# Kernel tuning notes

Hardware: AMD Instinct MI355X
Metric: run time of the kernel (lower is better)

Reference implementation:

```python
import jax, jax.numpy as jnp
import numpy as np

C_IN = 256
C_INTER = 128


def _pool_tv(a):
    # max-pool by 2 over the last two dims (t, v); kernel (1,2,2)
    *lead, t, v = a.shape
    return a.reshape(*lead, t // 2, 2, v // 2, 2).max(axis=(-3, -1))


def setup_inputs() -> dict:
    key = jax.random.key(0)
    ks = jax.random.split(key, 9)
    b, c, views, t, v = 8, 512, 4, 32, 32
    s = 1.0 / np.sqrt(C_IN)
    si = 1.0 / np.sqrt(C_INTER)
    return {
        "x": jax.random.normal(ks[0], (b, c, views, t, v), dtype=jnp.float32),
        "g_w": jax.random.normal(ks[1], (C_INTER, C_IN), dtype=jnp.float32) * s,
        "g_b": jax.random.normal(ks[2], (C_INTER,), dtype=jnp.float32) * s,
        "theta_w": jax.random.normal(ks[3], (C_INTER, C_IN), dtype=jnp.float32) * s,
        "theta_b": jax.random.normal(ks[4], (C_INTER,), dtype=jnp.float32) * s,
        "phi_w": jax.random.normal(ks[5], (C_INTER, C_IN), dtype=jnp.float32) * s,
        "phi_b": jax.random.normal(ks[6], (C_INTER,), dtype=jnp.float32) * s,
        "W_w": jax.random.normal(ks[7], (C_IN, C_INTER), dtype=jnp.float32) * si,
        "W_b": jax.random.normal(ks[8], (C_IN,), dtype=jnp.float32) * si,
    }


def reference(x, g_w, g_b, theta_w, theta_b, phi_w, phi_b, W_w, W_b):
    b, c, views, t, v = x.shape
    G = c // C_IN  # channel groups
    x5 = x.reshape(b, C_IN, G, views, t, v)
    x_pool = x5.mean(axis=2)  # (b, C_IN, views, t, v)

    # g branch: per-group 1x1 conv then (1,2,2) max-pool
    x_g = jnp.swapaxes(x5, 1, 2)  # (b, G, C_IN, views, t, v)
    g_full = jnp.einsum('bgcvtw,oc->bgovtw', x_g, g_w) + g_b[None, None, :, None, None, None]
    g_pooled = _pool_tv(g_full)  # (b, G, inter, views, t/2, v/2)
    M = views * (t // 2) * (v // 2)
    # (b, G, inter, M) -> (b, inter, G, M) -> (b, inter*G, M) -> (b, M, inter*G)
    g_x = jnp.swapaxes(g_pooled.reshape(b, G, C_INTER, M), 1, 2).reshape(b, C_INTER * G, M)
    g_x = jnp.swapaxes(g_x, 1, 2)

    # theta on full-resolution pooled-over-group x; phi subsampled
    N = views * t * v
    theta_x = jnp.einsum('bcvtw,oc->bovtw', x_pool, theta_w) + theta_b[None, :, None, None, None]
    theta_x = jnp.swapaxes(theta_x.reshape(b, C_INTER, N), 1, 2)  # (b, N, inter)
    phi_full = jnp.einsum('bcvtw,oc->bovtw', x_pool, phi_w) + phi_b[None, :, None, None, None]
    phi_x = _pool_tv(phi_full).reshape(b, C_INTER, M)  # (b, inter, M)

    f = jnp.einsum('bni,bim->bnm', theta_x, phi_x)  # (b, N, M)
    f_div_C = jax.nn.softmax(f, axis=-1)
    y = jnp.einsum('bnm,bmd->bnd', f_div_C, g_x)  # (b, N, inter*G)

    # (b, inter*G, N) -> (b, inter, G, views, t, v) -> (b, G, inter, ...)
    y = jnp.swapaxes(y, 1, 2).reshape(b, C_INTER, G, views, t, v)
    y = jnp.swapaxes(y, 1, 2)
    W_y = jnp.einsum('bgivtw,oi->bgovtw', y, W_w) + W_b[None, None, :, None, None, None]
    W_y = jnp.swapaxes(W_y, 1, 2).reshape(b, c, views, t, v)
    return W_y + x
```

## Files before the change

### kernel.cpp

```cpp
#include <hip/hip_runtime.h>

#define F_Y     0u
#define F_TH    4194304u
#define F_PHIB  6291456u
#define F_GB    6815744u

typedef __attribute__((ext_vector_type(4))) float f32x4;
typedef __attribute__((ext_vector_type(8))) short bf16x8;

__device__ __forceinline__ unsigned short f2bf(float f) {
  union { unsigned int i; float f; } x; x.f = f;
  unsigned int r = x.i + 0x7fffu + ((x.i >> 16) & 1u);
  return (unsigned short)(r >> 16);
}
__device__ __forceinline__ unsigned int pk2(float a, float b) {
  return (unsigned int)f2bf(a) | ((unsigned int)f2bf(b) << 16);
}
__device__ __forceinline__ void gload_lds16(const void* g, void* l) {
  __builtin_amdgcn_global_load_lds(
      (const __attribute__((address_space(1))) unsigned int*)g,
      (__attribute__((address_space(3))) unsigned int*)l, 16, 0, 0);
}

__global__ __launch_bounds__(512)
void k_front(const float* __restrict__ x,
             const float* __restrict__ tw, const float* __restrict__ tb,
             const float* __restrict__ pw, const float* __restrict__ pb,
             const float* __restrict__ gw, const float* __restrict__ gb,
             float* __restrict__ ws) {
  const int nt = blockIdx.x, b = blockIdx.y;
  const int n0 = nt * 128;
  const int tid = threadIdx.x;
  const int w = tid >> 6, lane = tid & 63, q = lane >> 4, col = lane & 15;

  __shared__ uint4 ldsb[5888];
  char* lds = (char*)ldsb;
  char* xs  = lds;
  char* Xm  = lds + 32768;
  char* Xg0 = lds + 43008;
  char* Xg1 = lds + 53248;
  char* Wt  = lds + 63488;
  char* Wp  = lds + 73728;
  char* Wg  = lds + 83968;

  f32x4 at[8], ap[8], a0[8], a1[8];
#pragma unroll
  for (int j = 0; j < 8; ++j) {
    at[j] = (f32x4){0.f, 0.f, 0.f, 0.f};
    ap[j] = (f32x4){0.f, 0.f, 0.f, 0.f};
    a0[j] = (f32x4){0.f, 0.f, 0.f, 0.f};
    a1[j] = (f32x4){0.f, 0.f, 0.f, 0.f};
  }

  for (int kc = 0; kc < 8; ++kc) {
    {
      const int ch = tid >> 5;
      const int so = (tid & 31) * 16;
#pragma unroll
      for (int i = 0; i < 4; ++i) {
        const int chh = 16 * i + ch;
        const float* src = x + ((size_t)(b * 512 + 64 * kc + chh)) * 4096 + n0;
        gload_lds16((const char*)src + (so ^ ((chh & 7) << 4)),
                    xs + 8192 * i + tid * 16);
      }
      const int o = tid >> 2, c4 = tid & 3;
      const size_t wo = (size_t)o * 256 + 32 * kc + 8 * c4;
      float4 t0 = ((const float4*)(tw + wo))[0], t1 = ((const float4*)(tw + wo))[1];
      float4 p0 = ((const float4*)(pw + wo))[0], p1 = ((const float4*)(pw + wo))[1];
      float4 g0 = ((const float4*)(gw + wo))[0], g1 = ((const float4*)(gw + wo))[1];
      *(uint4*)(Wt + o * 80 + 16 * c4) =
          make_uint4(pk2(t0.x, t0.y), pk2(t0.z, t0.w), pk2(t1.x, t1.y), pk2(t1.z, t1.w));
      *(uint4*)(Wp + o * 80 + 16 * c4) =
          make_uint4(pk2(p0.x, p0.y), pk2(p0.z, p0.w), pk2(p1.x, p1.y), pk2(p1.z, p1.w));
      *(uint4*)(Wg + o * 80 + 16 * c4) =
          make_uint4(pk2(g0.x, g0.y), pk2(g0.z, g0.w), pk2(g1.x, g1.y), pk2(g1.z, g1.w));
    }
    __syncthreads();
    {
      const int n = tid >> 2, c4 = tid & 3;
      unsigned um[4], u0[4], u1[4];
#pragma unroll
      for (int s = 0; s < 4; ++s) {
        float v[4];
#pragma unroll
        for (int e = 0; e < 2; ++e) {
          const int cp = 8 * c4 + 2 * s + e;
          const int l0 = 2 * cp, l1 = 2 * cp + 1;
          v[2 * e]     = *(const float*)(xs + l0 * 512 + ((n * 4) ^ ((l0 & 7) << 4)));
          v[2 * e + 1] = *(const float*)(xs + l1 * 512 + ((n * 4) ^ ((l1 & 7) << 4)));
        }
        um[s] = pk2(0.5f * (v[0] + v[1]), 0.5f * (v[2] + v[3]));
        u0[s] = pk2(v[0], v[2]);
        u1[s] = pk2(v[1], v[3]);
      }
      *(uint4*)(Xm  + n * 80 + 16 * c4) = make_uint4(um[0], um[1], um[2], um[3]);
      *(uint4*)(Xg0 + n * 80 + 16 * c4) = make_uint4(u0[0], u0[1], u0[2], u0[3]);
      *(uint4*)(Xg1 + n * 80 + 16 * c4) = make_uint4(u1[0], u1[1], u1[2], u1[3]);
    }
    __syncthreads();
    {
      const int ar = 16 * w + col;
      const bf16x8 aft = *(const bf16x8*)(Wt + ar * 80 + 16 * q);
      const bf16x8 afp = *(const bf16x8*)(Wp + ar * 80 + 16 * q);
      const bf16x8 afg = *(const bf16x8*)(Wg + ar * 80 + 16 * q);
#pragma unroll
      for (int j = 0; j < 8; ++j) {
        const int br = 16 * j + col;
        const bf16x8 bm = *(const bf16x8*)(Xm  + br * 80 + 16 * q);
        const bf16x8 b0 = *(const bf16x8*)(Xg0 + br * 80 + 16 * q);
        const bf16x8 b1 = *(const bf16x8*)(Xg1 + br * 80 + 16 * q);
        at[j] = __builtin_amdgcn_mfma_f32_16x16x32_bf16(aft, bm, at[j], 0, 0, 0);
        ap[j] = __builtin_amdgcn_mfma_f32_16x16x32_bf16(afp, bm, ap[j], 0, 0, 0);
        a0[j] = __builtin_amdgcn_mfma_f32_16x16x32_bf16(afg, b0, a0[j], 0, 0, 0);
        a1[j] = __builtin_amdgcn_mfma_f32_16x16x32_bf16(afg, b1, a1[j], 0, 0, 0);
      }
    }
    __syncthreads();
  }

  const int o0 = 16 * w + 4 * q;
  const int mb = (nt >> 3) * 256 + (nt & 7) * 32;

  {
    float bst[4];
#pragma unroll
    for (int r = 0; r < 4; ++r) bst[r] = tb[o0 + r];
#pragma unroll
    for (int j = 0; j < 8; ++j) {
      const int n = 16 * j + col;
      uint2 pkk = make_uint2(pk2(at[j][0] + bst[0], at[j][1] + bst[1]),
                             pk2(at[j][2] + bst[2], at[j][3] + bst[3]));
      *(uint2*)(xs + n * 256 + ((2 * o0) ^ ((n & 7) << 4))) = pkk;
    }
  }

  {
    float bsp[4];
#pragma unroll
    for (int r = 0; r < 4; ++r) bsp[r] = pb[o0 + r];
    unsigned short* phiB = (unsigned short*)(ws + F_PHIB);
#pragma unroll
    for (int jj = 0; jj < 4; ++jj) {
      const int j = (jj >> 1) * 4 + (jj & 1);
      f32x4 pm;
#pragma unroll
      for (int r = 0; r < 4; ++r) pm[r] = fmaxf(ap[j][r], ap[j + 2][r]);
#pragma unroll
      for (int r = 0; r < 4; ++r) pm[r] = fmaxf(pm[r], __shfl_xor(pm[r], 1));
      if ((col & 1) == 0) {
        const int vp = 8 * (j & 1) + (col >> 1);
        const int m = mb + 16 * (j >> 2) + vp;
        uint2 pkk = make_uint2(pk2(pm[0] + bsp[0], pm[1] + bsp[1]),
                               pk2(pm[2] + bsp[2], pm[3] + bsp[3]));
        *(uint2*)(phiB + ((size_t)(b * 1024) + m) * 128 + o0) = pkk;
      }
    }
  }

  {
    float bsg[4];
#pragma unroll
    for (int r = 0; r < 4; ++r) bsg[r] = gb[o0 + r];
#pragma unroll
    for (int gr = 0; gr < 2; ++gr) {
      char* pt = gr ? Xg1 : Xg0;
      const f32x4* ag = gr ? a1 : a0;
#pragma unroll
      for (int jj = 0; jj < 4; ++jj) {
        const int j = (jj >> 1) * 4 + (jj & 1);
        f32x4 pm;
#pragma unroll
        for (int r = 0; r < 4; ++r) pm[r] = fmaxf(ag[j][r], ag[j + 2][r]);
#pragma unroll
        for (int r = 0; r < 4; ++r) pm[r] = fmaxf(pm[r], __shfl_xor(pm[r], 1));
        if ((col & 1) == 0) {
          const int ml = 16 * (j >> 2) + 8 * (j & 1) + (col >> 1);
#pragma unroll
          for (int r = 0; r < 4; ++r)
            *(unsigned short*)(pt + (o0 + r) * 80 + ml * 2) = f2bf(pm[r] + bsg[r]);
        }
      }
    }
  }
  __syncthreads();

  {
    const int n = tid >> 2, seg = tid & 3;
    unsigned short* dst = (unsigned short*)(ws + F_TH) +
                          ((size_t)(b * 4096) + n0 + n) * 128 + seg * 32;
    const char* row = xs + n * 256;
    const int sw = (n & 7) << 4;
#pragma unroll
    for (int k = 0; k < 4; ++k)
      ((uint4*)dst)[k] = *(const uint4*)(row + ((64 * seg + 16 * k) ^ sw));
  }
  if (tid < 256) {
    const int o = tid >> 1, gr = tid & 1;
    const char* row = (gr ? Xg1 : Xg0) + o * 80;
    unsigned short* dst = (unsigned short*)(ws + F_GB) +
                          ((size_t)(b * 256) + 2 * o + gr) * 1024 + mb;
#pragma unroll
    for (int k = 0; k < 4; ++k)
      ((uint4*)dst)[k] = *(const uint4*)(row + 16 * k);
  }
}

#define NSIT 16
__global__ __launch_bounds__(512)
void k_attn_mfma(float* __restrict__ ws) {
  const int b = blockIdx.x;
  const int n0 = blockIdx.y * 128;
  const int tid = threadIdx.x;
  const int w = tid >> 6;
  const int lane = tid & 63;
  const int q = lane >> 4;
  const int col = lane & 15;
  const int ksw = (col & 7) << 4;

  __shared__ char lds[131072];
  char* plw0 = lds + 98304 + w * 4096;
  char* plw1 = plw0 + 2048;

  const unsigned short* thetaB = (const unsigned short*)(ws + F_TH);
  const char* phiBb = (const char*)((const unsigned short*)(ws + F_PHIB) + (size_t)b * 1024 * 128);
  const char* gBb   = (const char*)((const unsigned short*)(ws + F_GB) + (size_t)b * 256 * 1024);
  unsigned short* yB = (unsigned short*)(ws + F_Y);

  const int kr0 = lane >> 4;
  const int kso = (lane & 15) * 16;
  const int vr0 = lane >> 3;
  const int vso = (lane & 7) * 16;

  bf16x8 qf[4];
  {
    const unsigned short* qp = thetaB + ((size_t)(b * 4096 + n0 + 16 * w + col)) * 128 + 8 * q;
#pragma unroll
    for (int c = 0; c < 4; ++c) qf[c] = *(const bf16x8*)(qp + 32 * c);
  }

  f32x4 ot[16];
#pragma unroll
  for (int t = 0; t < 16; ++t) ot[t] = (f32x4){0.f, 0.f, 0.f, 0.f};
  float mrun = -1e30f, lsum = 0.f;

  {
    const int r = 4 * w + kr0;
    gload_lds16(phiBb + (size_t)r * 256 + (kso ^ ((r & 7) << 4)), lds + w * 1024);
    gload_lds16(phiBb + (size_t)(32 + r) * 256 + (kso ^ ((r & 7) << 4)),
                lds + 8192 + w * 1024);
#pragma unroll
    for (int j = 0; j < 4; ++j) {
      const int c = 4 * w + j;
      const int d = 8 * c + vr0;
      gload_lds16(gBb + (size_t)d * 2048 + (vso ^ ((d & 7) << 4)),
                  lds + 32768 + c * 1024);
    }
  }
  __syncthreads();

  for (int sit = 0; sit < NSIT; ++sit) {
    char* kt0 = lds + ((2 * sit) & 3) * 8192;
    char* kt1 = lds + ((2 * sit + 1) & 3) * 8192;
    char* vtc = lds + 32768 + (sit & 1) * 32768;

    if (sit + 1 < NSIT) {
      const int r = 4 * w + kr0;
      const int swk = (kso ^ ((r & 7) << 4));
      gload_lds16(phiBb + (size_t)((2 * sit + 2) * 32 + r) * 256 + swk,
                  lds + ((2 * sit + 2) & 3) * 8192 + w * 1024);
      gload_lds16(phiBb + (size_t)((2 * sit + 3) * 32 + r) * 256 + swk,
                  lds + ((2 * sit + 3) & 3) * 8192 + w * 1024);
      const size_t vm = (size_t)((sit + 1) * 64) * 2;
#pragma unroll
      for (int j = 0; j < 4; ++j) {
        const int c = 4 * w + j;
        const int d = 8 * c + vr0;
        gload_lds16(gBb + (size_t)d * 2048 + vm + (vso ^ ((d & 7) << 4)),
                    lds + 32768 + ((sit & 1) ^ 1) * 32768 + c * 1024);
      }
    }

    f32x4 st0[2], st1[2];
#pragma unroll
    for (int s = 0; s < 2; ++s) {
      st0[s] = (f32x4){0.f, 0.f, 0.f, 0.f};
      st1[s] = (f32x4){0.f, 0.f, 0.f, 0.f};
    }
    __builtin_amdgcn_s_setprio(1);
#pragma unroll
    for (int c = 0; c < 4; ++c)
#pragma unroll
      for (int s = 0; s < 2; ++s) {
        const bf16x8 kf0 = *(const bf16x8*)(kt0 + (16 * s + col) * 256 +
                                            ((64 * c + 16 * q) ^ ksw));
        const bf16x8 kf1 = *(const bf16x8*)(kt1 + (16 * s + col) * 256 +
                                            ((64 * c + 16 * q) ^ ksw));
        st0[s] = __builtin_amdgcn_mfma_f32_16x16x32_bf16(kf0, qf[c], st0[s], 0, 0, 0);
        st1[s] = __builtin_amdgcn_mfma_f32_16x16x32_bf16(kf1, qf[c], st1[s], 0, 0, 0);
      }
    __builtin_amdgcn_s_setprio(0);

    float pmax = -1e30f;
#pragma unroll
    for (int s = 0; s < 2; ++s)
#pragma unroll
      for (int r = 0; r < 4; ++r) {
        pmax = fmaxf(pmax, st0[s][r]);
        pmax = fmaxf(pmax, st1[s][r]);
      }
    pmax = fmaxf(pmax, __shfl_xor(pmax, 16));
    pmax = fmaxf(pmax, __shfl_xor(pmax, 32));
    if (!__all(pmax - mrun <= 8.f)) {
      const float mnew = fmaxf(mrun, pmax);
      const float scl = __expf(mrun - mnew);
      mrun = mnew;
      lsum *= scl;
#pragma unroll
      for (int t = 0; t < 16; ++t) {
        ot[t][0] *= scl; ot[t][1] *= scl; ot[t][2] *= scl; ot[t][3] *= scl;
      }
    }
    float rsum = 0.f;
#pragma unroll
    for (int s = 0; s < 2; ++s)
#pragma unroll
      for (int r = 0; r < 4; ++r) {
        st0[s][r] = __expf(st0[s][r] - mrun);
        st1[s][r] = __expf(st1[s][r] - mrun);
        rsum += st0[s][r] + st1[s][r];
      }
    rsum += __shfl_xor(rsum, 16);
    rsum += __shfl_xor(rsum, 32);
    lsum += rsum;

    char* prow0 = plw0 + col * 128;
    char* prow1 = plw1 + col * 128;
#pragma unroll
    for (int s = 0; s < 2; ++s)
#pragma unroll
      for (int hp = 0; hp < 2; ++hp) {
        *(unsigned int*)(prow0 + ((32 * s + 8 * q + 4 * hp) ^ ksw)) =
            pk2(st0[s][2 * hp], st0[s][2 * hp + 1]);
        *(unsigned int*)(prow1 + ((32 * s + 8 * q + 4 * hp) ^ ksw)) =
            pk2(st1[s][2 * hp], st1[s][2 * hp + 1]);
      }
    const bf16x8 pf0 = *(const bf16x8*)(prow0 + ((16 * q) ^ ksw));
    const bf16x8 pf1 = *(const bf16x8*)(prow1 + ((16 * q) ^ ksw));

    __builtin_amdgcn_s_setprio(1);
#pragma unroll
    for (int t = 0; t < 16; ++t) {
      const int d = 16 * t + col;
      const int dsw = (d & 7) << 4;
      const bf16x8 vf0 = *(const bf16x8*)(vtc + d * 128 + ((16 * q) ^ dsw));
      ot[t] = __builtin_amdgcn_mfma_f32_16x16x32_bf16(vf0, pf0, ot[t], 0, 0, 0);
    }
#pragma unroll
    for (int t = 0; t < 16; ++t) {
      const int d = 16 * t + col;
      const int dsw = (d & 7) << 4;
      const bf16x8 vf1 = *(const bf16x8*)(vtc + d * 128 + ((64 + 16 * q) ^ dsw));
      ot[t] = __builtin_amdgcn_mfma_f32_16x16x32_bf16(vf1, pf1, ot[t], 0, 0, 0);
    }
    __builtin_amdgcn_s_setprio(0);

    __syncthreads();
  }

  const float inv = 1.f / lsum;
  char* yt = lds;
  const int nl = 16 * w + col;
  const int swn = (nl & 7) << 4;
#pragma unroll
  for (int t = 0; t < 16; ++t) {
    const unsigned int w0 = pk2(ot[t][0] * inv, ot[t][2] * inv);
    const unsigned int w1 = pk2(ot[t][1] * inv, ot[t][3] * inv);
    const int bo = 16 * t + 4 * q;
    *(unsigned int*)(yt + nl * 256 + (bo ^ swn)) = w0;
    *(unsigned int*)(yt + (128 + nl) * 256 + (bo ^ swn)) = w1;
  }
  __syncthreads();
  {
    const int row = tid >> 1, h2 = tid & 1;
    const int gr = row >> 7, n = row & 127;
    unsigned short* dst = yB + (((size_t)(b * 2 + gr)) * 4096 + n0 + n) * 128 + h2 * 64;
    const char* srow = yt + row * 256;
    const int sw = (n & 7) << 4;
#pragma unroll
    for (int k = 0; k < 8; ++k)
      ((uint4*)dst)[k] = *(const uint4*)(srow + ((128 * h2 + 16 * k) ^ sw));
  }
}

__global__ __launch_bounds__(256)
void k_final_mfma(const float* __restrict__ x,
                  const float* __restrict__ Ww, const float* __restrict__ Wb,
                  const float* __restrict__ ws, float* __restrict__ out) {
  const int nt = blockIdx.x, gq = blockIdx.y, b = blockIdx.z;
  const int gr = gq & 1, ob = (gq >> 1) * 128;
  const int n0 = nt * 128;
  const int tid = threadIdx.x;
  const int w = tid >> 6, lane = tid & 63, q = lane >> 4, col = lane & 15;
  const unsigned short* yb = (const unsigned short*)(ws + F_Y);

  __shared__ uint4 ldsb[4096];
  char* As = (char*)ldsb;
  char* Bs = (char*)ldsb + 16384;

  f32x4 acc[2][8];
#pragma unroll
  for (int h = 0; h < 2; ++h)
#pragma unroll
    for (int j = 0; j < 8; ++j) acc[h][j] = (f32x4){0.f, 0.f, 0.f, 0.f};

  const int ro = tid >> 1, haf = tid & 1;
  for (int ks = 0; ks < 2; ++ks) {
    __syncthreads();
    {
      const float* src = Ww + (size_t)(ob + ro) * 128 + ks * 64 + haf * 32;
      char* row = As + ro * 128;
      const int sw = (ro & 7) << 4;
#pragma unroll
      for (int jj = 0; jj < 4; ++jj) {
        float4 a = ((const float4*)src)[2 * jj];
        float4 c4 = ((const float4*)src)[2 * jj + 1];
        uint4 pk;
        pk.x = pk2(a.x, a.y);  pk.y = pk2(a.z, a.w);
        pk.z = pk2(c4.x, c4.y); pk.w = pk2(c4.z, c4.w);
        *(uint4*)(row + ((haf * 64 + 16 * jj) ^ sw)) = pk;
      }
    }
    {
      const unsigned short* src = yb + (((size_t)(b * 2 + gr)) * 4096 + n0 + ro) * 128 + ks * 64 + haf * 32;
      char* row = Bs + ro * 128;
      const int sw = (ro & 7) << 4;
#pragma unroll
      for (int jj = 0; jj < 4; ++jj)
        *(uint4*)(row + ((haf * 64 + 16 * jj) ^ sw)) = ((const uint4*)src)[jj];
    }
    __syncthreads();
#pragma unroll
    for (int c = 0; c < 2; ++c) {
      bf16x8 af[2], bfr[8];
#pragma unroll
      for (int h = 0; h < 2; ++h) {
        const int r = 32 * w + 16 * h + col;
        af[h] = *(const bf16x8*)(As + r * 128 + ((64 * c + 16 * q) ^ ((r & 7) << 4)));
      }
#pragma unroll
      for (int j = 0; j < 8; ++j) {
        const int r = 16 * j + col;
        bfr[j] = *(const bf16x8*)(Bs + r * 128 + ((64 * c + 16 * q) ^ ((r & 7) << 4)));
      }
#pragma unroll
      for (int h = 0; h < 2; ++h)
#pragma unroll
        for (int j = 0; j < 8; ++j)
          acc[h][j] = __builtin_amdgcn_mfma_f32_16x16x32_bf16(af[h], bfr[j], acc[h][j], 0, 0, 0);
    }
  }

  __syncthreads();
  char* ft = (char*)ldsb;
#pragma unroll
  for (int h = 0; h < 2; ++h) {
    const int o0 = 32 * w + 16 * h + 4 * q;
#pragma unroll
    for (int j = 0; j < 8; ++j) {
      const int n = 16 * j + col;
#pragma unroll
      for (int r = 0; r < 4; ++r)
        *(float*)(ft + (o0 + r) * 512 + ((n * 4) ^ (((o0 + r) & 7) << 4))) = acc[h][j][r];
    }
  }
  __syncthreads();
  {
    const int o = tid >> 1, h2 = tid & 1;
    const float bsv = Wb[ob + o];
    const int ch = 2 * (ob + o) + gr;
    const size_t base = ((size_t)(b * 512 + ch)) * 4096 + n0 + h2 * 64;
    const char* row = ft + o * 512;
    const int sw = (o & 7) << 4;
#pragma unroll
    for (int k = 0; k < 16; ++k) {
      f32x4 v = *(const f32x4*)(row + ((256 * h2 + 16 * k) ^ sw));
      float4 xv = ((const float4*)(x + base))[k];
      ((float4*)(out + base))[k] = make_float4(v[0] + bsv + xv.x, v[1] + bsv + xv.y,
                                               v[2] + bsv + xv.z, v[3] + bsv + xv.w);
    }
  }
}

extern "C" void kernel_launch(void* const* d_in, const int* in_sizes, int n_in,
                              void* d_out, int out_size, void* d_ws, size_t ws_size,
                              hipStream_t stream) {
  const float* x  = (const float*)d_in[0];
  const float* gw = (const float*)d_in[1];
  const float* gb = (const float*)d_in[2];
  const float* tw = (const float*)d_in[3];
  const float* tb = (const float*)d_in[4];
  const float* pw = (const float*)d_in[5];
  const float* pb = (const float*)d_in[6];
  const float* Ww = (const float*)d_in[7];
  const float* Wb = (const float*)d_in[8];
  float* out = (float*)d_out;
  float* ws  = (float*)d_ws;

  k_front<<<dim3(32, 8), 512, 0, stream>>>(x, tw, tb, pw, pb, gw, gb, ws);
  k_attn_mfma<<<dim3(8, 32), 512, 0, stream>>>(ws);
  k_final_mfma<<<dim3(32, 4, 8), 256, 0, stream>>>(x, Ww, Wb, ws, out);
}
```

Measured before the change: 124.5 us.

## Fuse output W projection and residual into attention kernel epilogue

The final 1x1 W projection, bias and residual add move into the attention kernel's epilogue. The normalized y tile stays in LDS and each block multiplies it by W (read from global and converted to bf16 on the fly) with MFMA, then writes out+x directly. This removes the y workspace round trip and one kernel launch. In exchange the attention kernel carries 128 extra accumulator registers, which may reduce occupancy, and each block reloads the W weights from global memory without LDS staging.

```diff
diff --git a/kernel.cpp b/kernel.cpp
--- a/kernel.cpp
+++ b/kernel.cpp
@@ -1,9 +1,8 @@
 #include <hip/hip_runtime.h>
 
-#define F_Y     0u
-#define F_TH    4194304u
-#define F_PHIB  6291456u
-#define F_GB    6815744u
+#define F_TH    0u
+#define F_PHIB  2097152u
+#define F_GB    2621440u
 
 typedef __attribute__((ext_vector_type(4))) float f32x4;
 typedef __attribute__((ext_vector_type(8))) short bf16x8;
@@ -207,7 +206,9 @@
 
 #define NSIT 16
 __global__ __launch_bounds__(512)
-void k_attn_mfma(float* __restrict__ ws) {
+void k_attn_mfma(const float* __restrict__ x,
+                 const float* __restrict__ Ww, const float* __restrict__ Wb,
+                 float* __restrict__ ws, float* __restrict__ out) {
   const int b = blockIdx.x;
   const int n0 = blockIdx.y * 128;
   const int tid = threadIdx.x;
@@ -224,7 +225,6 @@
   const unsigned short* thetaB = (const unsigned short*)(ws + F_TH);
   const char* phiBb = (const char*)((const unsigned short*)(ws + F_PHIB) + (size_t)b * 1024 * 128);
   const char* gBb   = (const char*)((const unsigned short*)(ws + F_GB) + (size_t)b * 256 * 1024);
-  unsigned short* yB = (unsigned short*)(ws + F_Y);
 
   const int kr0 = lane >> 4;
   const int kso = (lane & 15) * 16;
@@ -369,125 +369,87 @@
 
   const float inv = 1.f / lsum;
   char* yt = lds;
-  const int nl = 16 * w + col;
-  const int swn = (nl & 7) << 4;
-#pragma unroll
-  for (int t = 0; t < 16; ++t) {
-    const unsigned int w0 = pk2(ot[t][0] * inv, ot[t][2] * inv);
-    const unsigned int w1 = pk2(ot[t][1] * inv, ot[t][3] * inv);
-    const int bo = 16 * t + 4 * q;
-    *(unsigned int*)(yt + nl * 256 + (bo ^ swn)) = w0;
-    *(unsigned int*)(yt + (128 + nl) * 256 + (bo ^ swn)) = w1;
+  {
+    const int nl = 16 * w + col;
+    const int swn = (nl & 7) << 4;
+#pragma unroll
+    for (int t = 0; t < 16; ++t) {
+      const unsigned int w0 = pk2(ot[t][0] * inv, ot[t][2] * inv);
+      const unsigned int w1 = pk2(ot[t][1] * inv, ot[t][3] * inv);
+      const int bo = 16 * t + 4 * q;
+      *(unsigned int*)(yt + nl * 256 + (bo ^ swn)) = w0;
+      *(unsigned int*)(yt + (128 + nl) * 256 + (bo ^ swn)) = w1;
+    }
   }
   __syncthreads();
-  {
-    const int row = tid >> 1, h2 = tid & 1;
-    const int gr = row >> 7, n = row & 127;
-    unsigned short* dst = yB + (((size_t)(b * 2 + gr)) * 4096 + n0 + n) * 128 + h2 * 64;
-    const char* srow = yt + row * 256;
-    const int sw = (n & 7) << 4;
-#pragma unroll
-    for (int k = 0; k < 8; ++k)
-      ((uint4*)dst)[k] = *(const uint4*)(srow + ((128 * h2 + 16 * k) ^ sw));
-  }
-}
-
-__global__ __launch_bounds__(256)
-void k_final_mfma(const float* __restrict__ x,
-                  const float* __restrict__ Ww, const float* __restrict__ Wb,
-                  const float* __restrict__ ws, float* __restrict__ out) {
-  const int nt = blockIdx.x, gq = blockIdx.y, b = blockIdx.z;
-  const int gr = gq & 1, ob = (gq >> 1) * 128;
-  const int n0 = nt * 128;
-  const int tid = threadIdx.x;
-  const int w = tid >> 6, lane = tid & 63, q = lane >> 4, col = lane & 15;
-  const unsigned short* yb = (const unsigned short*)(ws + F_Y);
-
-  __shared__ uint4 ldsb[4096];
-  char* As = (char*)ldsb;
-  char* Bs = (char*)ldsb + 16384;
-
-  f32x4 acc[2][8];
-#pragma unroll
-  for (int h = 0; h < 2; ++h)
-#pragma unroll
-    for (int j = 0; j < 8; ++j) acc[h][j] = (f32x4){0.f, 0.f, 0.f, 0.f};
-
-  const int ro = tid >> 1, haf = tid & 1;
-  for (int ks = 0; ks < 2; ++ks) {
+
+  f32x4 facc[2][2][8];
+#pragma unroll
+  for (int gr = 0; gr < 2; ++gr)
+#pragma unroll
+    for (int h = 0; h < 2; ++h)
+#pragma unroll
+      for (int j = 0; j < 8; ++j) facc[gr][h][j] = (f32x4){0.f, 0.f, 0.f, 0.f};
+
+#pragma unroll
+  for (int gr = 0; gr < 2; ++gr) {
+#pragma unroll
+    for (int c = 0; c < 4; ++c) {
+      bf16x8 bfr[8];
+#pragma unroll
+      for (int j = 0; j < 8; ++j) {
+        const int nl = 16 * j + col;
+        bfr[j] = *(const bf16x8*)(yt + (128 * gr + nl) * 256 + ((64 * c + 16 * q) ^ ksw));
+      }
+#pragma unroll
+      for (int h = 0; h < 2; ++h) {
+        const int o = 32 * w + 16 * h + col;
+        const float* wp = Ww + (size_t)o * 128 + 32 * c + 8 * q;
+        const float4 w0 = ((const float4*)wp)[0];
+        const float4 w1 = ((const float4*)wp)[1];
+        union { unsigned u[4]; bf16x8 v; } af;
+        af.u[0] = pk2(w0.x, w0.y); af.u[1] = pk2(w0.z, w0.w);
+        af.u[2] = pk2(w1.x, w1.y); af.u[3] = pk2(w1.z, w1.w);
+#pragma unroll
+        for (int j = 0; j < 8; ++j)
+          facc[gr][h][j] = __builtin_amdgcn_mfma_f32_16x16x32_bf16(af.v, bfr[j], facc[gr][h][j], 0, 0, 0);
+      }
+    }
+  }
+  __syncthreads();
+
+  char* ft = lds;
+#pragma unroll
+  for (int gr = 0; gr < 2; ++gr) {
+#pragma unroll
+    for (int h = 0; h < 2; ++h) {
+      const int o0 = 32 * w + 16 * h + 4 * q;
+#pragma unroll
+      for (int j = 0; j < 8; ++j) {
+        const int n = 16 * j + col;
+#pragma unroll
+        for (int r = 0; r < 4; ++r)
+          *(float*)(ft + (o0 + r) * 512 + ((n * 4) ^ (((o0 + r) & 7) << 4))) =
+              facc[gr][h][j][r];
+      }
+    }
     __syncthreads();
     {
-      const float* src = Ww + (size_t)(ob + ro) * 128 + ks * 64 + haf * 32;
-      char* row = As + ro * 128;
-      const int sw = (ro & 7) << 4;
-#pragma unroll
-      for (int jj = 0; jj < 4; ++jj) {
-        float4 a = ((const float4*)src)[2 * jj];
-        float4 c4 = ((const float4*)src)[2 * jj + 1];
-        uint4 pk;
-        pk.x = pk2(a.x, a.y);  pk.y = pk2(a.z, a.w);
-        pk.z = pk2(c4.x, c4.y); pk.w = pk2(c4.z, c4.w);
-        *(uint4*)(row + ((haf * 64 + 16 * jj) ^ sw)) = pk;
-      }
-    }
-    {
-      const unsigned short* src = yb + (((size_t)(b * 2 + gr)) * 4096 + n0 + ro) * 128 + ks * 64 + haf * 32;
-      char* row = Bs + ro * 128;
-      const int sw = (ro & 7) << 4;
-#pragma unroll
-      for (int jj = 0; jj < 4; ++jj)
-        *(uint4*)(row + ((haf * 64 + 16 * jj) ^ sw)) = ((const uint4*)src)[jj];
-    }
-    __syncthreads();
-#pragma unroll
-    for (int c = 0; c < 2; ++c) {
-      bf16x8 af[2], bfr[8];
-#pragma unroll
-      for (int h = 0; h < 2; ++h) {
-        const int r = 32 * w + 16 * h + col;
-        af[h] = *(const bf16x8*)(As + r * 128 + ((64 * c + 16 * q) ^ ((r & 7) << 4)));
-      }
-#pragma unroll
-      for (int j = 0; j < 8; ++j) {
-        const int r = 16 * j + col;
-        bfr[j] = *(const bf16x8*)(Bs + r * 128 + ((64 * c + 16 * q) ^ ((r & 7) << 4)));
-      }
-#pragma unroll
-      for (int h = 0; h < 2; ++h)
-#pragma unroll
-        for (int j = 0; j < 8; ++j)
-          acc[h][j] = __builtin_amdgcn_mfma_f32_16x16x32_bf16(af[h], bfr[j], acc[h][j], 0, 0, 0);
-    }
-  }
-
-  __syncthreads();
-  char* ft = (char*)ldsb;
-#pragma unroll
-  for (int h = 0; h < 2; ++h) {
-    const int o0 = 32 * w + 16 * h + 4 * q;
-#pragma unroll
-    for (int j = 0; j < 8; ++j) {
-      const int n = 16 * j + col;
-#pragma unroll
-      for (int r = 0; r < 4; ++r)
-        *(float*)(ft + (o0 + r) * 512 + ((n * 4) ^ (((o0 + r) & 7) << 4))) = acc[h][j][r];
-    }
-  }
-  __syncthreads();
-  {
-    const int o = tid >> 1, h2 = tid & 1;
-    const float bsv = Wb[ob + o];
-    const int ch = 2 * (ob + o) + gr;
-    const size_t base = ((size_t)(b * 512 + ch)) * 4096 + n0 + h2 * 64;
-    const char* row = ft + o * 512;
-    const int sw = (o & 7) << 4;
-#pragma unroll
-    for (int k = 0; k < 16; ++k) {
-      f32x4 v = *(const f32x4*)(row + ((256 * h2 + 16 * k) ^ sw));
-      float4 xv = ((const float4*)(x + base))[k];
-      ((float4*)(out + base))[k] = make_float4(v[0] + bsv + xv.x, v[1] + bsv + xv.y,
-                                               v[2] + bsv + xv.z, v[3] + bsv + xv.w);
-    }
+      const int o = tid >> 1, h2 = tid & 1;
+      const float bsv = Wb[o];
+      const int ch = 2 * o + gr;
+      const size_t base = ((size_t)(b * 512 + ch)) * 4096 + n0 + h2 * 64;
+      const char* row = ft + o * 512;
+      const int sw = (o & 7) << 4;
+#pragma unroll
+      for (int k = 0; k < 16; ++k) {
+        f32x4 v = *(const f32x4*)(row + ((256 * h2 + 16 * k) ^ sw));
+        float4 xv = ((const float4*)(x + base))[k];
+        ((float4*)(out + base))[k] = make_float4(v[0] + bsv + xv.x, v[1] + bsv + xv.y,
+                                                 v[2] + bsv + xv.z, v[3] + bsv + xv.w);
+      }
+    }
+    if (gr == 0) __syncthreads();
   }
 }
 
@@ -507,6 +469,5 @@
   float* ws  = (float*)d_ws;
 
   k_front<<<dim3(32, 8), 512, 0, stream>>>(x, tw, tb, pw, pb, gw, gb, ws);
-  k_attn_mfma<<<dim3(8, 32), 512, 0, stream>>>(ws);
-  k_final_mfma<<<dim3(32, 4, 8), 256, 0, stream>>>(x, Ww, Wb, ws, out);
-}
+  k_attn_mfma<<<dim3(8, 32), 512, 0, stream>>>(x, Ww, Wb, ws, out);
+}
```

Measured after the change: 108.5 us. -12.8%, faster.
